# Kernel tuning notes

Hardware: AMD Instinct MI355X
Metric: run time of the kernel (lower is better)

The kernel has to match this reference:

```python
import jax, jax.numpy as jnp
import numpy as np

N = 1024
H = 1024
B, T = 64, 256


def setup_inputs() -> dict:
    key = jax.random.key(0)
    ks = jax.random.split(key, 12)
    inp = {
        "h_time": jax.random.normal(ks[0], (B, T, H), dtype=jnp.float32),
        "A_pearson": jax.random.uniform(ks[1], (N, N), dtype=jnp.float32),
        "E_dyn": jax.random.normal(ks[2], (N, H), dtype=jnp.float32) * 0.1,
        "alpha_raw": jnp.float32(0.5),
        "tau_raw": jnp.float32(1.0),
        # gate_gen: Linear(H, H//2) -> GELU -> Linear(H//2, N) -> Sigmoid
        "gate_W1": jax.random.normal(ks[3], (H, H // 2), dtype=jnp.float32) * (1.0 / np.sqrt(H)),
        "gate_b1": jnp.zeros((H // 2,), dtype=jnp.float32),
        "gate_W2": jax.random.normal(ks[4], (H // 2, N), dtype=jnp.float32) * (1.0 / np.sqrt(H // 2)),
        "gate_b2": jnp.zeros((N,), dtype=jnp.float32),
        "h2n_W": jax.random.normal(ks[5], (H, N), dtype=jnp.float32) * (1.0 / np.sqrt(H)),
        "h2n_b": jnp.zeros((N,), dtype=jnp.float32),
        "n2h_W": jax.random.normal(ks[6], (N, H), dtype=jnp.float32) * (1.0 / np.sqrt(N)),
        "n2h_b": jnp.zeros((H,), dtype=jnp.float32),
        "ln_w": jnp.ones((H,), dtype=jnp.float32),
        "ln_b": jnp.zeros((H,), dtype=jnp.float32),
    }
    return inp


def _layernorm(x, w, b, eps=1e-5):
    mu = x.mean(-1, keepdims=True)
    var = ((x - mu) ** 2).mean(-1, keepdims=True)
    return (x - mu) * jax.lax.rsqrt(var + eps) * w + b


def reference(h_time, A_pearson, E_dyn, alpha_raw, tau_raw,
              gate_W1, gate_b1, gate_W2, gate_b2,
              h2n_W, h2n_b, n2h_W, n2h_b, ln_w, ln_b):
    tau = jax.nn.softplus(tau_raw) + 1e-6
    alpha = jax.nn.sigmoid(alpha_raw)

    h_mean = h_time.mean(axis=(0, 1))                      # [H]
    E = E_dyn + h_mean[None, :]
    E_cur = E / jnp.maximum(jnp.linalg.norm(E, axis=-1, keepdims=True), 1e-12)  # F.normalize

    A_dyn = jax.nn.relu(E_cur @ E_cur.T)                   # [N,N]
    A_dyn = A_dyn / (A_dyn.sum(axis=-1, keepdims=True) + 1e-6)
    A_dyn = 0.5 * (A_dyn + A_dyn.T)
    A_base = alpha * A_pearson + (1.0 - alpha) * A_dyn

    h_gate = h_time.mean(axis=1)                           # [B,H]
    hid = jax.nn.gelu(h_gate @ gate_W1 + gate_b1, approximate=False)
    gamma = jax.nn.sigmoid(hid @ gate_W2 + gate_b2)        # [B,N]

    # Python loop over batch == row-scaling by mean gate
    A_mix = A_base * gamma.mean(axis=0)[:, None]           # [N,N]

    z_nodes = h_time @ h2n_W + h2n_b                       # [B,T,N]
    z_gcn = jnp.einsum('btn,mn->btm', z_nodes, A_mix)      # z_nodes @ A_mix.T
    msg_h = z_gcn @ n2h_W + n2h_b                          # [B,T,H]

    logits = (A_base @ E_cur) / tau                        # [N,H]
    node_attn = jax.nn.softmax(logits, axis=0)
    global_w = jnp.tanh(node_attn.mean(axis=0))            # [H]

    y = h_time * (1.0 + global_w) + msg_h
    return _layernorm(y, ln_w, ln_b)
```

## Files before the change

### kernel.cpp

```cpp
#include <hip/hip_runtime.h>
#include <math.h>

#define H 1024
#define Nn 1024
#define Bb 64
#define Tt 256
#define BT (Bb * Tt)

typedef unsigned short ushort_t;
typedef __attribute__((ext_vector_type(8))) short bf16x8;
typedef __attribute__((ext_vector_type(4))) float f32x4;


__device__ __forceinline__ ushort_t f2bf(float x) {
    union { float f; unsigned u; } v; v.f = x;
    unsigned r = v.u + 0x7FFFu + ((v.u >> 16) & 1u);
    return (ushort_t)(r >> 16);
}
__device__ __forceinline__ float bf2f(ushort_t h) {
    union { unsigned u; float f; } v; v.u = ((unsigned)h) << 16; return v.f;
}

__device__ __forceinline__ float block_reduce_sum_256(float v) {
    __shared__ float sbuf[4];
    __syncthreads();
    #pragma unroll
    for (int off = 32; off > 0; off >>= 1) v += __shfl_down(v, off, 64);
    int lane = threadIdx.x & 63, w = threadIdx.x >> 6;
    if (lane == 0) sbuf[w] = v;
    __syncthreads();
    if (threadIdx.x == 0) sbuf[0] = sbuf[0] + sbuf[1] + sbuf[2] + sbuf[3];
    __syncthreads();
    return sbuf[0];
}


__global__ void k_hgate(const float* __restrict__ h_time, float* __restrict__ h_gate,
                        ushort_t* __restrict__ ht_bf16, const float* __restrict__ n2h_b,
                        float* __restrict__ rowsumS, float* __restrict__ bias_h) {
    int b = blockIdx.y;
    int col = blockIdx.x * 256 + threadIdx.x;
    if (b == 0) {
        rowsumS[col] = 0.f;
        bias_h[col] = n2h_b[col];
    }
    float s = 0.f;
    const size_t base = (size_t)b * Tt * H + col;
    for (int t = 0; t < Tt; ++t) {
        float v = h_time[base + (size_t)t * H];
        s += v;
        ht_bf16[base + (size_t)t * H] = f2bf(v);
    }
    h_gate[b * H + col] = s * (1.0f / Tt);
}

__global__ void k_hmean(const float* __restrict__ h_gate, float* __restrict__ h_mean) {
    int h = blockIdx.x * 256 + threadIdx.x;
    float s = 0.f;
    for (int b = 0; b < Bb; ++b) s += h_gate[b * H + h];
    h_mean[h] = s * (1.0f / Bb);
}

__global__ void k_ecur(const float* __restrict__ E_dyn, const float* __restrict__ h_mean,
                       ushort_t* __restrict__ E_b) {
    int n = blockIdx.x;
    float e[4]; float ss = 0.f;
    #pragma unroll
    for (int q = 0; q < 4; ++q) {
        int h = threadIdx.x + 256 * q;
        e[q] = E_dyn[(size_t)n * H + h] + h_mean[h];
        ss += e[q] * e[q];
    }
    float tot = block_reduce_sum_256(ss);
    float scale = 1.0f / fmaxf(sqrtf(tot), 1e-12f);
    #pragma unroll
    for (int q = 0; q < 4; ++q) {
        int h = threadIdx.x + 256 * q;
        E_b[(size_t)n * H + h] = f2bf(e[q] * scale);
    }
}

__global__ void k_prepW(const float* __restrict__ n2h_W, const float* __restrict__ h2n_W,
                        const float* __restrict__ W1, const float* __restrict__ W2,
                        ushort_t* __restrict__ n2hWT_h, ushort_t* __restrict__ n2hWT_l,
                        ushort_t* __restrict__ h2nW_h, ushort_t* __restrict__ h2nW_l,
                        float* __restrict__ W1T, float* __restrict__ W2T) {
    __shared__ float tile[32][33];
    int id = blockIdx.x;
    int tx = threadIdx.x & 31, ty = threadIdx.x >> 5;
    if (id < 1024) {
        int i0 = (id >> 5) * 32, j0 = (id & 31) * 32;
        #pragma unroll
        for (int q = 0; q < 4; ++q)
            tile[ty + 8 * q][tx] = n2h_W[(size_t)(i0 + ty + 8 * q) * H + j0 + tx];
        __syncthreads();
        #pragma unroll
        for (int q = 0; q < 4; ++q) {
            float v = tile[tx][ty + 8 * q];
            size_t o = (size_t)(j0 + ty + 8 * q) * Nn + i0 + tx;
            ushort_t hh = f2bf(v);
            n2hWT_h[o] = hh;
            n2hWT_l[o] = f2bf(v - bf2f(hh));
        }
    } else if (id < 2048) {
        size_t idx = (size_t)(id - 1024) * 1024 + threadIdx.x * 4;
        float4 v = *(const float4*)&h2n_W[idx];
        float c[4] = {v.x, v.y, v.z, v.w};
        union { ushort_t u[4]; uint2 w; } ph, pl;
        #pragma unroll
        for (int q = 0; q < 4; ++q) {
            ph.u[q] = f2bf(c[q]);
            pl.u[q] = f2bf(c[q] - bf2f(ph.u[q]));
        }
        *(uint2*)&h2nW_h[idx] = ph.w;
        *(uint2*)&h2nW_l[idx] = pl.w;
    } else if (id < 2560) {
        int t = id - 2048;
        int i0 = (t >> 4) * 32, j0 = (t & 15) * 32;
        #pragma unroll
        for (int q = 0; q < 4; ++q)
            tile[ty + 8 * q][tx] = W1[(size_t)(i0 + ty + 8 * q) * 512 + j0 + tx];
        __syncthreads();
        #pragma unroll
        for (int q = 0; q < 4; ++q)
            W1T[(size_t)(j0 + ty + 8 * q) * 1024 + i0 + tx] = tile[tx][ty + 8 * q];
    } else {
        int t = id - 2560;
        int i0 = (t >> 5) * 32, j0 = (t & 31) * 32;
        #pragma unroll
        for (int q = 0; q < 4; ++q)
            tile[ty + 8 * q][tx] = W2[(size_t)(i0 + ty + 8 * q) * 1024 + j0 + tx];
        __syncthreads();
        #pragma unroll
        for (int q = 0; q < 4; ++q)
            W2T[(size_t)(j0 + ty + 8 * q) * 512 + i0 + tx] = tile[tx][ty + 8 * q];
    }
}

__global__ __launch_bounds__(256) void k_mlp1(const float* __restrict__ h_gate,
                                              const float* __restrict__ W1T,
                                              const float* __restrict__ b1,
                                              float* __restrict__ hid) {
    int gid = blockIdx.x * 4 + (threadIdx.x >> 6);
    int lane = threadIdx.x & 63;
    int b = gid >> 9, j = gid & 511;
    const float* xr = h_gate + b * H;
    const float* wr = W1T + (size_t)j * H;
    float s = 0.f;
    #pragma unroll
    for (int it = 0; it < 4; ++it) {
        int k = it * 256 + lane * 4;
        float4 x4 = *(const float4*)&xr[k];
        float4 w4 = *(const float4*)&wr[k];
        s += x4.x * w4.x + x4.y * w4.y + x4.z * w4.z + x4.w * w4.w;
    }
    #pragma unroll
    for (int off = 32; off > 0; off >>= 1) s += __shfl_down(s, off, 64);
    if (lane == 0) {
        float a = s + b1[j];
        hid[b * 512 + j] = 0.5f * a * (1.0f + erff(a * 0.70710678118654752f));
    }
}

__global__ __launch_bounds__(256) void k_mlp2(const float* __restrict__ hid,
                                              const float* __restrict__ W2T,
                                              const float* __restrict__ b2,
                                              float* __restrict__ gmean) {
    int n = blockIdx.x * 4 + (threadIdx.x >> 6);
    int lane = threadIdx.x & 63;
    const float* wr = W2T + (size_t)n * 512;
    float4 w0 = *(const float4*)&wr[lane * 4];
    float4 w1 = *(const float4*)&wr[256 + lane * 4];
    float bb = b2[n];
    float acc = 0.f;
    for (int b = 0; b < Bb; ++b) {
        const float* xr = hid + b * 512;
        float4 x0 = *(const float4*)&xr[lane * 4];
        float4 x1 = *(const float4*)&xr[256 + lane * 4];
        float s = x0.x * w0.x + x0.y * w0.y + x0.z * w0.z + x0.w * w0.w
                + x1.x * w1.x + x1.y * w1.y + x1.z * w1.z + x1.w * w1.w;
        #pragma unroll
        for (int off = 32; off > 0; off >>= 1) s += __shfl_down(s, off, 64);
        if (lane == 0) acc += 1.0f / (1.0f + expf(-(s + bb)));
    }
    if (lane == 0) gmean[n] = acc * (1.0f / Bb);
}

__global__ void k_amixT(const ushort_t* __restrict__ Sb, const float* __restrict__ A_p,
                        const float* __restrict__ rowsumS, const float* __restrict__ gmean,
                        const float* __restrict__ alpha_raw,
                        ushort_t* __restrict__ Th, ushort_t* __restrict__ Tl) {
    __shared__ float tile[32][33];
    int i0 = blockIdx.y * 32, j0 = blockIdx.x * 32;
    int tx = threadIdx.x & 31, ty = threadIdx.x >> 5;
    float alpha = 1.0f / (1.0f + expf(-alpha_raw[0]));
    #pragma unroll
    for (int q = 0; q < 4; ++q) {
        int i = i0 + ty + 8 * q, j = j0 + tx;
        size_t idx = (size_t)i * Nn + j;
        float s = bf2f(Sb[idx]);
        float ad = 0.5f * s * (1.0f / (rowsumS[i] + 1e-6f) + 1.0f / (rowsumS[j] + 1e-6f));
        tile[ty + 8 * q][tx] = gmean[i] * fmaf(alpha, A_p[idx], (1.0f - alpha) * ad);
    }
    __syncthreads();
    #pragma unroll
    for (int q = 0; q < 4; ++q) {
        float v = tile[tx][ty + 8 * q];
        size_t o = (size_t)(j0 + ty + 8 * q) * Nn + i0 + tx;
        ushort_t hh = f2bf(v);
        Th[o] = hh;
        Tl[o] = f2bf(v - bf2f(hh));
    }
}

template <int PASSES, int EPI>
__global__ __launch_bounds__(256) void gemm64_bt(
    const ushort_t* __restrict__ Ah, const ushort_t* __restrict__ Al,
    const ushort_t* __restrict__ Bh, const ushort_t* __restrict__ Bl,
    ushort_t* __restrict__ O1, ushort_t* __restrict__ O2,
    float* __restrict__ fout, const float* __restrict__ fvec,
    int M, int N, int K) {
    constexpr int NST = (PASSES == 3) ? 4 : 2;
    __shared__ ushort_t sStage[NST * 64 * 32];
    ushort_t* sAh = sStage;
    ushort_t* sBh = sStage + 64 * 32;
    ushort_t* sAl = sStage + (NST == 4 ? 2 * 64 * 32 : 0);
    ushort_t* sBl = sStage + (NST == 4 ? 3 * 64 * 32 : 0);
    const int tid = threadIdx.x, wave = tid >> 6, lane = tid & 63;
    const int quad = lane >> 4, l16 = lane & 15;
    const int m0 = blockIdx.y * 64, n0 = blockIdx.x * 64;
    const int wm = (wave >> 1) * 32, wn = (wave & 1) * 32;

    f32x4 acc[2][2];
    #pragma unroll
    for (int i = 0; i < 2; ++i)
        #pragma unroll
        for (int j = 0; j < 2; ++j)
            acc[i][j] = (f32x4){0.f, 0.f, 0.f, 0.f};

    for (int k0 = 0; k0 < K; k0 += 32) {
        __syncthreads();
        {
            const int row = tid >> 2, q = tid & 3;
            const size_t offA = (size_t)(m0 + row) * K + k0 + q * 8;
            const size_t offB = (size_t)(n0 + row) * K + k0 + q * 8;
            __builtin_amdgcn_global_load_lds(
                (const __attribute__((address_space(1))) unsigned int*)(Ah + offA),
                (__attribute__((address_space(3))) unsigned int*)&sAh[tid * 8], 16, 0, 0);
            __builtin_amdgcn_global_load_lds(
                (const __attribute__((address_space(1))) unsigned int*)(Bh + offB),
                (__attribute__((address_space(3))) unsigned int*)&sBh[tid * 8], 16, 0, 0);
            if constexpr (PASSES == 3) {
                __builtin_amdgcn_global_load_lds(
                    (const __attribute__((address_space(1))) unsigned int*)(Al + offA),
                    (__attribute__((address_space(3))) unsigned int*)&sAl[tid * 8], 16, 0, 0);
                __builtin_amdgcn_global_load_lds(
                    (const __attribute__((address_space(1))) unsigned int*)(Bl + offB),
                    (__attribute__((address_space(3))) unsigned int*)&sBl[tid * 8], 16, 0, 0);
            }
        }
        __syncthreads();
        bf16x8 fah[2], fbh[2];
        bf16x8 fal[PASSES == 3 ? 2 : 1], fbl[PASSES == 3 ? 2 : 1];
        #pragma unroll
        for (int i = 0; i < 2; ++i) {
            fah[i] = *(const bf16x8*)&sAh[(wm + i * 16 + l16) * 32 + quad * 8];
            fbh[i] = *(const bf16x8*)&sBh[(wn + i * 16 + l16) * 32 + quad * 8];
            if constexpr (PASSES == 3) {
                fal[i] = *(const bf16x8*)&sAl[(wm + i * 16 + l16) * 32 + quad * 8];
                fbl[i] = *(const bf16x8*)&sBl[(wn + i * 16 + l16) * 32 + quad * 8];
            }
        }
        #pragma unroll
        for (int i = 0; i < 2; ++i)
            #pragma unroll
            for (int j = 0; j < 2; ++j) {
                acc[i][j] = __builtin_amdgcn_mfma_f32_16x16x32_bf16(fah[i], fbh[j], acc[i][j], 0, 0, 0);
                if constexpr (PASSES == 3) {
                    acc[i][j] = __builtin_amdgcn_mfma_f32_16x16x32_bf16(fah[i], fbl[j], acc[i][j], 0, 0, 0);
                    acc[i][j] = __builtin_amdgcn_mfma_f32_16x16x32_bf16(fal[i], fbh[j], acc[i][j], 0, 0, 0);
                }
            }
    }

    float fv[2];
    if constexpr (EPI == 2) {
        #pragma unroll
        for (int j = 0; j < 2; ++j) fv[j] = fvec[n0 + wn + j * 16 + l16];
    }
    #pragma unroll
    for (int i = 0; i < 2; ++i)
        #pragma unroll
        for (int r = 0; r < 4; ++r) {
            const int m = m0 + wm + i * 16 + quad * 4 + r;
            float rowacc = 0.f;
            #pragma unroll
            for (int j = 0; j < 2; ++j) {
                const size_t o = (size_t)m * N + n0 + wn + j * 16 + l16;
                float v = acc[i][j][r];
                if constexpr (EPI == 1) {
                    v = fmaxf(v, 0.f);
                    O1[o] = f2bf(v);
                    rowacc += v;
                } else if constexpr (EPI == 2) {
                    ushort_t hh = f2bf(v);
                    O1[o] = hh;
                    O2[o] = f2bf(v - bf2f(hh));
                    rowacc += v * fv[j];
                } else {
                    O1[o] = f2bf(v);
                }
            }
            if constexpr (EPI == 1 || EPI == 2) {
                rowacc += __shfl_xor(rowacc, 1);
                rowacc += __shfl_xor(rowacc, 2);
                rowacc += __shfl_xor(rowacc, 4);
                rowacc += __shfl_xor(rowacc, 8);
                if (l16 == 0) atomicAdd(&fout[m], rowacc);
            }
        }
}

__global__ __launch_bounds__(256) void gemm_big(
    const ushort_t* __restrict__ A, const ushort_t* __restrict__ Bt,
    float* __restrict__ fout, const float* __restrict__ fvec,
    int M, int N, int K) {
    __shared__ ushort_t sStage[2 * 128 * 32];
    ushort_t* sAh = sStage;
    ushort_t* sBh = sStage + 128 * 32;

    const int tid = threadIdx.x;
    const int wave = tid >> 6, lane = tid & 63;
    const int quad = lane >> 4, l16 = lane & 15;
    int bx = blockIdx.x, g = bx & 7, s = bx >> 3;
    const int m0 = (g * 16 + (s >> 3)) * 128;
    const int n0 = (s & 7) * 128;
    const int wm = (wave >> 1) * 64, wn = (wave & 1) * 64;

    f32x4 acc[4][4];
    #pragma unroll
    for (int i = 0; i < 4; ++i)
        #pragma unroll
        for (int j = 0; j < 4; ++j)
            acc[i][j] = (f32x4){0.f, 0.f, 0.f, 0.f};

    for (int k0 = 0; k0 < K; k0 += 32) {
        __syncthreads();
        #pragma unroll
        for (int inst = 0; inst < 2; ++inst) {
            const int cbase = (wave * 2 + inst) * 64;
            const int c = cbase + lane;
            const int row = c >> 2, q = c & 3;
            const size_t offA = (size_t)(m0 + row) * K + k0 + q * 8;
            const size_t offB = (size_t)(n0 + row) * K + k0 + q * 8;
            __builtin_amdgcn_global_load_lds(
                (const __attribute__((address_space(1))) unsigned int*)(A + offA),
                (__attribute__((address_space(3))) unsigned int*)&sAh[cbase * 8], 16, 0, 0);
            __builtin_amdgcn_global_load_lds(
                (const __attribute__((address_space(1))) unsigned int*)(Bt + offB),
                (__attribute__((address_space(3))) unsigned int*)&sBh[cbase * 8], 16, 0, 0);
        }
        __syncthreads();
        bf16x8 fah[4], fbh[4];
        #pragma unroll
        for (int i = 0; i < 4; ++i) {
            fah[i] = *(const bf16x8*)&sAh[(wm + i * 16 + l16) * 32 + quad * 8];
            fbh[i] = *(const bf16x8*)&sBh[(wn + i * 16 + l16) * 32 + quad * 8];
        }
        #pragma unroll
        for (int i = 0; i < 4; ++i)
            #pragma unroll
            for (int j = 0; j < 4; ++j)
                acc[i][j] = __builtin_amdgcn_mfma_f32_16x16x32_bf16(fah[i], fbh[j], acc[i][j], 0, 0, 0);
    }
    __syncthreads();

    float* EsW = (float*)sStage + wave * (16 * 64);
    const float SC = 1.0009765622f;

    #pragma unroll
    for (int i = 0; i < 4; ++i) {
        #pragma unroll
        for (int j = 0; j < 4; ++j)
            #pragma unroll
            for (int r = 0; r < 4; ++r)
                EsW[(quad * 4 + r) * 64 + j * 16 + l16] = acc[i][j][r];
        __syncthreads();
        #pragma unroll
        for (int it = 0; it < 4; ++it) {
            const int idx = it * 64 + lane;
            const int row = idx >> 4, f4 = idx & 15;
            const int m = m0 + wm + i * 16 + row;
            const int coln = n0 + wn + f4 * 4;
            float4 v = *(const float4*)&EsW[row * 64 + f4 * 4];
            float4 b4 = *(const float4*)&fvec[coln];
            ushort4 h4 = *(const ushort4*)&A[(size_t)m * N + coln];
            float4 y;
            y.x = v.x + b4.x + SC * bf2f(h4.x);
            y.y = v.y + b4.y + SC * bf2f(h4.y);
            y.z = v.z + b4.z + SC * bf2f(h4.z);
            y.w = v.w + b4.w + SC * bf2f(h4.w);
            *(float4*)&fout[(size_t)m * N + coln] = y;
        }
        __syncthreads();
    }
}

__global__ void k_final_ln(const float* __restrict__ ln_w, const float* __restrict__ ln_b,
                           float* __restrict__ out) {
    size_t base = (size_t)blockIdx.x * H;
    int t4 = threadIdx.x * 4;
    float4 y4 = *(const float4*)&out[base + t4];
    float mu = block_reduce_sum_256(y4.x + y4.y + y4.z + y4.w) * (1.0f / H);
    float dx = y4.x - mu, dy = y4.y - mu, dz = y4.z - mu, dw = y4.w - mu;
    float var = block_reduce_sum_256(dx * dx + dy * dy + dz * dz + dw * dw) * (1.0f / H);
    float rstd = rsqrtf(var + 1e-5f);
    float4 w4 = *(const float4*)&ln_w[t4];
    float4 b4 = *(const float4*)&ln_b[t4];
    float4 o;
    o.x = fmaf(dx * rstd, w4.x, b4.x);
    o.y = fmaf(dy * rstd, w4.y, b4.y);
    o.z = fmaf(dz * rstd, w4.z, b4.z);
    o.w = fmaf(dw * rstd, w4.w, b4.w);
    *(float4*)&out[base + t4] = o;
}


extern "C" void kernel_launch(void* const* d_in, const int* in_sizes, int n_in,
                              void* d_out, int out_size, void* d_ws, size_t ws_size,
                              hipStream_t stream) {
    const float* h_time    = (const float*)d_in[0];
    const float* A_p       = (const float*)d_in[1];
    const float* E_dyn     = (const float*)d_in[2];
    const float* alpha_raw = (const float*)d_in[3];
    const float* gW1   = (const float*)d_in[5];
    const float* gb1   = (const float*)d_in[6];
    const float* gW2   = (const float*)d_in[7];
    const float* gb2   = (const float*)d_in[8];
    const float* h2n_W = (const float*)d_in[9];
    const float* h2n_b = (const float*)d_in[10];
    const float* n2h_W = (const float*)d_in[11];
    const float* n2h_b = (const float*)d_in[12];
    const float* ln_w  = (const float*)d_in[13];
    const float* ln_b  = (const float*)d_in[14];
    float* out = (float*)d_out;

    float* ws = (float*)d_ws;
    float* h_gate  = ws;  ws += Bb * H;
    float* h_mean  = ws;  ws += H;
    float* rowsumS = ws;  ws += Nn;
    float* bias_h  = ws;  ws += H;
    float* hid     = ws;  ws += Bb * 512;
    float* gmean   = ws;  ws += Nn;
    float* W1T     = ws;  ws += 512 * H;
    float* W2T     = ws;  ws += H * 512;
    ws += 256;
    ushort_t* E_b     = (ushort_t*)ws;  ws += (Nn * H) / 2;
    ushort_t* Sb      = (ushort_t*)ws;  ws += (Nn * Nn) / 2;
    ushort_t* AmixT_h = (ushort_t*)ws;  ws += (Nn * Nn) / 2;
    ushort_t* AmixT_l = (ushort_t*)ws;  ws += (Nn * Nn) / 2;
    ushort_t* n2hWT_h = (ushort_t*)ws;  ws += (Nn * H) / 2;
    ushort_t* n2hWT_l = (ushort_t*)ws;  ws += (Nn * H) / 2;
    ushort_t* h2nW_h  = (ushort_t*)ws;  ws += (H * Nn) / 2;
    ushort_t* h2nW_l  = (ushort_t*)ws;  ws += (H * Nn) / 2;
    ushort_t* C1Th    = (ushort_t*)ws;  ws += (H * Nn) / 2;
    ushort_t* C1Tl    = (ushort_t*)ws;  ws += (H * Nn) / 2;
    ushort_t* C2t     = (ushort_t*)ws;  ws += (H * H) / 2;
    ushort_t* ht      = (ushort_t*)ws;  ws += ((size_t)BT * H) / 2;

    k_hgate<<<dim3(4, 64), 256, 0, stream>>>(h_time, h_gate, ht, n2h_b, rowsumS, bias_h);
    k_prepW<<<3072, 256, 0, stream>>>(n2h_W, h2n_W, gW1, gW2,
                                      n2hWT_h, n2hWT_l, h2nW_h, h2nW_l, W1T, W2T);
    k_hmean<<<4, 256, 0, stream>>>(h_gate, h_mean);
    k_ecur<<<1024, 256, 0, stream>>>(E_dyn, h_mean, E_b);
    k_mlp1<<<8192, 256, 0, stream>>>(h_gate, W1T, gb1, hid);
    k_mlp2<<<256, 256, 0, stream>>>(hid, W2T, gb2, gmean);
    gemm64_bt<1, 1><<<dim3(16, 16), 256, 0, stream>>>(
        E_b, nullptr, E_b, nullptr, Sb, nullptr, rowsumS, nullptr, Nn, Nn, H);
    k_amixT<<<dim3(32, 32), 256, 0, stream>>>(Sb, A_p, rowsumS, gmean, alpha_raw, AmixT_h, AmixT_l);
    gemm64_bt<3, 2><<<dim3(16, 16), 256, 0, stream>>>(
        n2hWT_h, n2hWT_l, AmixT_h, AmixT_l, C1Th, C1Tl, bias_h, h2n_b, Nn, Nn, Nn);
    gemm64_bt<3, 3><<<dim3(16, 16), 256, 0, stream>>>(
        C1Th, C1Tl, h2nW_h, h2nW_l, C2t, nullptr, nullptr, nullptr, Nn, Nn, Nn);
    gemm_big<<<1024, 256, 0, stream>>>(ht, C2t, out, bias_h, BT, H, H);
    k_final_ln<<<BT, 256, 0, stream>>>(ln_w, ln_b, out);
}
```

Before: 366.2 us.

## Merge small prep kernels, widen GEMM K-tile to 64, warp-per-row layernorm

Several independent prep kernels are merged into multi-role launches (h_time stats with weight prep, E normalization with MLP1, MLP2 with the similarity GEMM). The h_time reduction is split across 8 time chunks so more blocks share the work. Both GEMMs now stage 64-wide K tiles in shared memory, halving the number of barrier and load rounds at the cost of more LDS per block. The final layernorm handles one row per wavefront with shuffle reductions instead of block-level shared memory. Together these aim to cut launch overhead, raise parallelism in the bandwidth-bound prep, and reduce sync cost, but the larger LDS footprint may lower occupancy.

Result: faster. 346.6 us (-5.4%).

```diff
diff --git a/kernel.cpp b/kernel.cpp
--- a/kernel.cpp
+++ b/kernel.cpp
@@ -34,62 +34,39 @@
     return sbuf[0];
 }
 
-
-__global__ void k_hgate(const float* __restrict__ h_time, float* __restrict__ h_gate,
-                        ushort_t* __restrict__ ht_bf16, const float* __restrict__ n2h_b,
-                        float* __restrict__ rowsumS, float* __restrict__ bias_h) {
-    int b = blockIdx.y;
-    int col = blockIdx.x * 256 + threadIdx.x;
-    if (b == 0) {
-        rowsumS[col] = 0.f;
-        bias_h[col] = n2h_b[col];
-    }
-    float s = 0.f;
-    const size_t base = (size_t)b * Tt * H + col;
-    for (int t = 0; t < Tt; ++t) {
-        float v = h_time[base + (size_t)t * H];
-        s += v;
-        ht_bf16[base + (size_t)t * H] = f2bf(v);
-    }
-    h_gate[b * H + col] = s * (1.0f / Tt);
-}
-
-__global__ void k_hmean(const float* __restrict__ h_gate, float* __restrict__ h_mean) {
-    int h = blockIdx.x * 256 + threadIdx.x;
-    float s = 0.f;
-    for (int b = 0; b < Bb; ++b) s += h_gate[b * H + h];
-    h_mean[h] = s * (1.0f / Bb);
-}
-
-__global__ void k_ecur(const float* __restrict__ E_dyn, const float* __restrict__ h_mean,
-                       ushort_t* __restrict__ E_b) {
-    int n = blockIdx.x;
-    float e[4]; float ss = 0.f;
-    #pragma unroll
-    for (int q = 0; q < 4; ++q) {
-        int h = threadIdx.x + 256 * q;
-        e[q] = E_dyn[(size_t)n * H + h] + h_mean[h];
-        ss += e[q] * e[q];
-    }
-    float tot = block_reduce_sum_256(ss);
-    float scale = 1.0f / fmaxf(sqrtf(tot), 1e-12f);
-    #pragma unroll
-    for (int q = 0; q < 4; ++q) {
-        int h = threadIdx.x + 256 * q;
-        E_b[(size_t)n * H + h] = f2bf(e[q] * scale);
-    }
-}
-
-__global__ void k_prepW(const float* __restrict__ n2h_W, const float* __restrict__ h2n_W,
-                        const float* __restrict__ W1, const float* __restrict__ W2,
-                        ushort_t* __restrict__ n2hWT_h, ushort_t* __restrict__ n2hWT_l,
-                        ushort_t* __restrict__ h2nW_h, ushort_t* __restrict__ h2nW_l,
-                        float* __restrict__ W1T, float* __restrict__ W2T) {
+__global__ void k_stage1(const float* __restrict__ h_time, float* __restrict__ hg_part,
+                         ushort_t* __restrict__ ht_bf16, const float* __restrict__ n2h_b,
+                         float* __restrict__ rowsumS, float* __restrict__ bias_h,
+                         const float* __restrict__ n2h_W, const float* __restrict__ h2n_W,
+                         const float* __restrict__ W1, const float* __restrict__ W2,
+                         ushort_t* __restrict__ n2hWT_h, ushort_t* __restrict__ n2hWT_l,
+                         ushort_t* __restrict__ h2nW_h, ushort_t* __restrict__ h2nW_l,
+                         float* __restrict__ W1T, float* __restrict__ W2T) {
     __shared__ float tile[32][33];
     int id = blockIdx.x;
+    if (id < 2048) {
+        int b = id >> 5, r = id & 31;
+        int z = r >> 2, cb = r & 3;
+        int col = cb * 256 + threadIdx.x;
+        if (b == 0 && z == 0) {
+            rowsumS[col] = 0.f;
+            bias_h[col] = n2h_b[col];
+        }
+        float s = 0.f;
+        #pragma unroll 4
+        for (int t = z * 32; t < z * 32 + 32; ++t) {
+            size_t o = ((size_t)b * Tt + t) * H + col;
+            float v = h_time[o];
+            s += v;
+            ht_bf16[o] = f2bf(v);
+        }
+        hg_part[(size_t)(b * 8 + z) * H + col] = s;
+        return;
+    }
     int tx = threadIdx.x & 31, ty = threadIdx.x >> 5;
-    if (id < 1024) {
-        int i0 = (id >> 5) * 32, j0 = (id & 31) * 32;
+    if (id < 3072) {
+        int t = id - 2048;
+        int i0 = (t >> 5) * 32, j0 = (t & 31) * 32;
         #pragma unroll
         for (int q = 0; q < 4; ++q)
             tile[ty + 8 * q][tx] = n2h_W[(size_t)(i0 + ty + 8 * q) * H + j0 + tx];
@@ -102,8 +79,8 @@
             n2hWT_h[o] = hh;
             n2hWT_l[o] = f2bf(v - bf2f(hh));
         }
-    } else if (id < 2048) {
-        size_t idx = (size_t)(id - 1024) * 1024 + threadIdx.x * 4;
+    } else if (id < 4096) {
+        size_t idx = (size_t)(id - 3072) * 1024 + threadIdx.x * 4;
         float4 v = *(const float4*)&h2n_W[idx];
         float c[4] = {v.x, v.y, v.z, v.w};
         union { ushort_t u[4]; uint2 w; } ph, pl;
@@ -114,8 +91,8 @@
         }
         *(uint2*)&h2nW_h[idx] = ph.w;
         *(uint2*)&h2nW_l[idx] = pl.w;
-    } else if (id < 2560) {
-        int t = id - 2048;
+    } else if (id < 4608) {
+        int t = id - 4096;
         int i0 = (t >> 4) * 32, j0 = (t & 15) * 32;
         #pragma unroll
         for (int q = 0; q < 4; ++q)
@@ -125,7 +102,7 @@
         for (int q = 0; q < 4; ++q)
             W1T[(size_t)(j0 + ty + 8 * q) * 1024 + i0 + tx] = tile[tx][ty + 8 * q];
     } else {
-        int t = id - 2560;
+        int t = id - 4608;
         int i0 = (t >> 5) * 32, j0 = (t & 31) * 32;
         #pragma unroll
         for (int q = 0; q < 4; ++q)
@@ -137,11 +114,48 @@
     }
 }
 
-__global__ __launch_bounds__(256) void k_mlp1(const float* __restrict__ h_gate,
-                                              const float* __restrict__ W1T,
-                                              const float* __restrict__ b1,
-                                              float* __restrict__ hid) {
-    int gid = blockIdx.x * 4 + (threadIdx.x >> 6);
+__global__ void k_stage2(const float* __restrict__ hg_part, float* __restrict__ h_gate,
+                         float* __restrict__ h_mean) {
+    int id = blockIdx.x;
+    if (id < 256) {
+        int b = id >> 2, cb = id & 3;
+        int col = cb * 256 + threadIdx.x;
+        float s = 0.f;
+        #pragma unroll
+        for (int z = 0; z < 8; ++z) s += hg_part[(size_t)(b * 8 + z) * H + col];
+        h_gate[b * H + col] = s * (1.0f / Tt);
+    } else {
+        int h = (id - 256) * 256 + threadIdx.x;
+        float s = 0.f;
+        for (int r = 0; r < 512; ++r) s += hg_part[(size_t)r * H + h];
+        h_mean[h] = s * (1.0f / (Bb * Tt));
+    }
+}
+
+__global__ __launch_bounds__(256) void k_stage3(
+    const float* __restrict__ E_dyn, const float* __restrict__ h_mean,
+    ushort_t* __restrict__ E_b,
+    const float* __restrict__ h_gate, const float* __restrict__ W1T,
+    const float* __restrict__ b1, float* __restrict__ hid) {
+    if (blockIdx.x < 1024) {
+        int n = blockIdx.x;
+        float e[4]; float ss = 0.f;
+        #pragma unroll
+        for (int q = 0; q < 4; ++q) {
+            int h = threadIdx.x + 256 * q;
+            e[q] = E_dyn[(size_t)n * H + h] + h_mean[h];
+            ss += e[q] * e[q];
+        }
+        float tot = block_reduce_sum_256(ss);
+        float scale = 1.0f / fmaxf(sqrtf(tot), 1e-12f);
+        #pragma unroll
+        for (int q = 0; q < 4; ++q) {
+            int h = threadIdx.x + 256 * q;
+            E_b[(size_t)n * H + h] = f2bf(e[q] * scale);
+        }
+        return;
+    }
+    int gid = (blockIdx.x - 1024) * 4 + (threadIdx.x >> 6);
     int lane = threadIdx.x & 63;
     int b = gid >> 9, j = gid & 511;
     const float* xr = h_gate + b * H;
@@ -162,73 +176,23 @@
     }
 }
 
-__global__ __launch_bounds__(256) void k_mlp2(const float* __restrict__ hid,
-                                              const float* __restrict__ W2T,
-                                              const float* __restrict__ b2,
-                                              float* __restrict__ gmean) {
-    int n = blockIdx.x * 4 + (threadIdx.x >> 6);
-    int lane = threadIdx.x & 63;
-    const float* wr = W2T + (size_t)n * 512;
-    float4 w0 = *(const float4*)&wr[lane * 4];
-    float4 w1 = *(const float4*)&wr[256 + lane * 4];
-    float bb = b2[n];
-    float acc = 0.f;
-    for (int b = 0; b < Bb; ++b) {
-        const float* xr = hid + b * 512;
-        float4 x0 = *(const float4*)&xr[lane * 4];
-        float4 x1 = *(const float4*)&xr[256 + lane * 4];
-        float s = x0.x * w0.x + x0.y * w0.y + x0.z * w0.z + x0.w * w0.w
-                + x1.x * w1.x + x1.y * w1.y + x1.z * w1.z + x1.w * w1.w;
-        #pragma unroll
-        for (int off = 32; off > 0; off >>= 1) s += __shfl_down(s, off, 64);
-        if (lane == 0) acc += 1.0f / (1.0f + expf(-(s + bb)));
-    }
-    if (lane == 0) gmean[n] = acc * (1.0f / Bb);
-}
-
-__global__ void k_amixT(const ushort_t* __restrict__ Sb, const float* __restrict__ A_p,
-                        const float* __restrict__ rowsumS, const float* __restrict__ gmean,
-                        const float* __restrict__ alpha_raw,
-                        ushort_t* __restrict__ Th, ushort_t* __restrict__ Tl) {
-    __shared__ float tile[32][33];
-    int i0 = blockIdx.y * 32, j0 = blockIdx.x * 32;
-    int tx = threadIdx.x & 31, ty = threadIdx.x >> 5;
-    float alpha = 1.0f / (1.0f + expf(-alpha_raw[0]));
-    #pragma unroll
-    for (int q = 0; q < 4; ++q) {
-        int i = i0 + ty + 8 * q, j = j0 + tx;
-        size_t idx = (size_t)i * Nn + j;
-        float s = bf2f(Sb[idx]);
-        float ad = 0.5f * s * (1.0f / (rowsumS[i] + 1e-6f) + 1.0f / (rowsumS[j] + 1e-6f));
-        tile[ty + 8 * q][tx] = gmean[i] * fmaf(alpha, A_p[idx], (1.0f - alpha) * ad);
-    }
-    __syncthreads();
-    #pragma unroll
-    for (int q = 0; q < 4; ++q) {
-        float v = tile[tx][ty + 8 * q];
-        size_t o = (size_t)(j0 + ty + 8 * q) * Nn + i0 + tx;
-        ushort_t hh = f2bf(v);
-        Th[o] = hh;
-        Tl[o] = f2bf(v - bf2f(hh));
-    }
-}
-
 template <int PASSES, int EPI>
-__global__ __launch_bounds__(256) void gemm64_bt(
+__device__ __forceinline__ void gemm64_body(
+    int bx, int by,
     const ushort_t* __restrict__ Ah, const ushort_t* __restrict__ Al,
     const ushort_t* __restrict__ Bh, const ushort_t* __restrict__ Bl,
     ushort_t* __restrict__ O1, ushort_t* __restrict__ O2,
     float* __restrict__ fout, const float* __restrict__ fvec,
     int M, int N, int K) {
     constexpr int NST = (PASSES == 3) ? 4 : 2;
-    __shared__ ushort_t sStage[NST * 64 * 32];
+    __shared__ ushort_t sStage[NST * 64 * 64];
     ushort_t* sAh = sStage;
-    ushort_t* sBh = sStage + 64 * 32;
-    ushort_t* sAl = sStage + (NST == 4 ? 2 * 64 * 32 : 0);
-    ushort_t* sBl = sStage + (NST == 4 ? 3 * 64 * 32 : 0);
+    ushort_t* sBh = sStage + 64 * 64;
+    ushort_t* sAl = sStage + (NST == 4 ? 2 * 64 * 64 : 0);
+    ushort_t* sBl = sStage + (NST == 4 ? 3 * 64 * 64 : 0);
     const int tid = threadIdx.x, wave = tid >> 6, lane = tid & 63;
     const int quad = lane >> 4, l16 = lane & 15;
-    const int m0 = blockIdx.y * 64, n0 = blockIdx.x * 64;
+    const int m0 = by * 64, n0 = bx * 64;
     const int wm = (wave >> 1) * 32, wn = (wave & 1) * 32;
 
     f32x4 acc[2][2];
@@ -238,49 +202,56 @@
         for (int j = 0; j < 2; ++j)
             acc[i][j] = (f32x4){0.f, 0.f, 0.f, 0.f};
 
-    for (int k0 = 0; k0 < K; k0 += 32) {
-        __syncthreads();
-        {
-            const int row = tid >> 2, q = tid & 3;
+    for (int k0 = 0; k0 < K; k0 += 64) {
+        __syncthreads();
+        #pragma unroll
+        for (int inst = 0; inst < 2; ++inst) {
+            const int cbase = (wave * 2 + inst) * 64;
+            const int c = cbase + lane;
+            const int row = c >> 3, q = c & 7;
             const size_t offA = (size_t)(m0 + row) * K + k0 + q * 8;
             const size_t offB = (size_t)(n0 + row) * K + k0 + q * 8;
             __builtin_amdgcn_global_load_lds(
                 (const __attribute__((address_space(1))) unsigned int*)(Ah + offA),
-                (__attribute__((address_space(3))) unsigned int*)&sAh[tid * 8], 16, 0, 0);
+                (__attribute__((address_space(3))) unsigned int*)&sAh[cbase * 8], 16, 0, 0);
             __builtin_amdgcn_global_load_lds(
                 (const __attribute__((address_space(1))) unsigned int*)(Bh + offB),
-                (__attribute__((address_space(3))) unsigned int*)&sBh[tid * 8], 16, 0, 0);
+                (__attribute__((address_space(3))) unsigned int*)&sBh[cbase * 8], 16, 0, 0);
             if constexpr (PASSES == 3) {
                 __builtin_amdgcn_global_load_lds(
                     (const __attribute__((address_space(1))) unsigned int*)(Al + offA),
-                    (__attribute__((address_space(3))) unsigned int*)&sAl[tid * 8], 16, 0, 0);
+                    (__attribute__((address_space(3))) unsigned int*)&sAl[cbase * 8], 16, 0, 0);
                 __builtin_amdgcn_global_load_lds(
                     (const __attribute__((address_space(1))) unsigned int*)(Bl + offB),
-                    (__attribute__((address_space(3))) unsigned int*)&sBl[tid * 8], 16, 0, 0);
+                    (__attribute__((address_space(3))) unsigned int*)&sBl[cbase * 8], 16, 0, 0);
             }
         }
         __syncthreads();
-        bf16x8 fah[2], fbh[2];
-        bf16x8 fal[PASSES == 3 ? 2 : 1], fbl[PASSES == 3 ? 2 : 1];
-        #pragma unroll
-        for (int i = 0; i < 2; ++i) {
-            fah[i] = *(const bf16x8*)&sAh[(wm + i * 16 + l16) * 32 + quad * 8];
-            fbh[i] = *(const bf16x8*)&sBh[(wn + i * 16 + l16) * 32 + quad * 8];
-            if constexpr (PASSES == 3) {
-                fal[i] = *(const bf16x8*)&sAl[(wm + i * 16 + l16) * 32 + quad * 8];
-                fbl[i] = *(const bf16x8*)&sBl[(wn + i * 16 + l16) * 32 + quad * 8];
-            }
-        }
-        #pragma unroll
-        for (int i = 0; i < 2; ++i)
-            #pragma unroll
-            for (int j = 0; j < 2; ++j) {
-                acc[i][j] = __builtin_amdgcn_mfma_f32_16x16x32_bf16(fah[i], fbh[j], acc[i][j], 0, 0, 0);
+        #pragma unroll
+        for (int half = 0; half < 2; ++half) {
+            bf16x8 fah[2], fbh[2];
+            bf16x8 fal[PASSES == 3 ? 2 : 1], fbl[PASSES == 3 ? 2 : 1];
+            #pragma unroll
+            for (int i = 0; i < 2; ++i) {
+                const int ko = half * 32 + quad * 8;
+                fah[i] = *(const bf16x8*)&sAh[(wm + i * 16 + l16) * 64 + ko];
+                fbh[i] = *(const bf16x8*)&sBh[(wn + i * 16 + l16) * 64 + ko];
                 if constexpr (PASSES == 3) {
-                    acc[i][j] = __builtin_amdgcn_mfma_f32_16x16x32_bf16(fah[i], fbl[j], acc[i][j], 0, 0, 0);
-                    acc[i][j] = __builtin_amdgcn_mfma_f32_16x16x32_bf16(fal[i], fbh[j], acc[i][j], 0, 0, 0);
+                    fal[i] = *(const bf16x8*)&sAl[(wm + i * 16 + l16) * 64 + ko];
+                    fbl[i] = *(const bf16x8*)&sBl[(wn + i * 16 + l16) * 64 + ko];
                 }
             }
+            #pragma unroll
+            for (int i = 0; i < 2; ++i)
+                #pragma unroll
+                for (int j = 0; j < 2; ++j) {
+                    acc[i][j] = __builtin_amdgcn_mfma_f32_16x16x32_bf16(fah[i], fbh[j], acc[i][j], 0, 0, 0);
+                    if constexpr (PASSES == 3) {
+                        acc[i][j] = __builtin_amdgcn_mfma_f32_16x16x32_bf16(fah[i], fbl[j], acc[i][j], 0, 0, 0);
+                        acc[i][j] = __builtin_amdgcn_mfma_f32_16x16x32_bf16(fal[i], fbh[j], acc[i][j], 0, 0, 0);
+                    }
+                }
+        }
     }
 
     float fv[2];
@@ -321,13 +292,87 @@
         }
 }
 
+__global__ __launch_bounds__(256) void k_stage4(
+    const float* __restrict__ hid, const float* __restrict__ W2T,
+    const float* __restrict__ b2, float* __restrict__ gmean,
+    const ushort_t* __restrict__ E_b, ushort_t* __restrict__ Sb,
+    float* __restrict__ rowsumS) {
+    if (blockIdx.x < 256) {
+        int n = blockIdx.x * 4 + (threadIdx.x >> 6);
+        int lane = threadIdx.x & 63;
+        const float* wr = W2T + (size_t)n * 512;
+        float4 w0 = *(const float4*)&wr[lane * 4];
+        float4 w1 = *(const float4*)&wr[256 + lane * 4];
+        float bb = b2[n];
+        float acc = 0.f;
+        for (int b = 0; b < Bb; ++b) {
+            const float* xr = hid + b * 512;
+            float4 x0 = *(const float4*)&xr[lane * 4];
+            float4 x1 = *(const float4*)&xr[256 + lane * 4];
+            float s = x0.x * w0.x + x0.y * w0.y + x0.z * w0.z + x0.w * w0.w
+                    + x1.x * w1.x + x1.y * w1.y + x1.z * w1.z + x1.w * w1.w;
+            #pragma unroll
+            for (int off = 32; off > 0; off >>= 1) s += __shfl_down(s, off, 64);
+            if (lane == 0) acc += 1.0f / (1.0f + expf(-(s + bb)));
+        }
+        if (lane == 0) gmean[n] = acc * (1.0f / Bb);
+        return;
+    }
+    int t = blockIdx.x - 256;
+    gemm64_body<1, 1>(t & 15, t >> 4, E_b, nullptr, E_b, nullptr,
+                      Sb, nullptr, rowsumS, nullptr, Nn, Nn, H);
+}
+
+__global__ void k_amixT(const ushort_t* __restrict__ Sb, const float* __restrict__ A_p,
+                        const float* __restrict__ rowsumS, const float* __restrict__ gmean,
+                        const float* __restrict__ alpha_raw,
+                        ushort_t* __restrict__ Th, ushort_t* __restrict__ Tl) {
+    __shared__ float tile[32][33];
+    int i0 = blockIdx.y * 32, j0 = blockIdx.x * 32;
+    int tx = threadIdx.x & 31, ty = threadIdx.x >> 5;
+    float alpha = 1.0f / (1.0f + expf(-alpha_raw[0]));
+    #pragma unroll
+    for (int q = 0; q < 4; ++q) {
+        int i = i0 + ty + 8 * q, j = j0 + tx;
+        size_t idx = (size_t)i * Nn + j;
+        float s = bf2f(Sb[idx]);
+        float ad = 0.5f * s * (1.0f / (rowsumS[i] + 1e-6f) + 1.0f / (rowsumS[j] + 1e-6f));
+        tile[ty + 8 * q][tx] = gmean[i] * fmaf(alpha, A_p[idx], (1.0f - alpha) * ad);
+    }
+    __syncthreads();
+    #pragma unroll
+    for (int q = 0; q < 4; ++q) {
+        float v = tile[tx][ty + 8 * q];
+        size_t o = (size_t)(j0 + ty + 8 * q) * Nn + i0 + tx;
+        ushort_t hh = f2bf(v);
+        Th[o] = hh;
+        Tl[o] = f2bf(v - bf2f(hh));
+    }
+}
+
+__global__ __launch_bounds__(256) void k_c1t(
+    const ushort_t* __restrict__ Ah, const ushort_t* __restrict__ Al,
+    const ushort_t* __restrict__ Bh, const ushort_t* __restrict__ Bl,
+    ushort_t* __restrict__ O1, ushort_t* __restrict__ O2,
+    float* __restrict__ fout, const float* __restrict__ fvec) {
+    gemm64_body<3, 2>(blockIdx.x & 15, blockIdx.x >> 4, Ah, Al, Bh, Bl, O1, O2, fout, fvec,
+                      Nn, Nn, Nn);
+}
+__global__ __launch_bounds__(256) void k_c2t(
+    const ushort_t* __restrict__ Ah, const ushort_t* __restrict__ Al,
+    const ushort_t* __restrict__ Bh, const ushort_t* __restrict__ Bl,
+    ushort_t* __restrict__ O1) {
+    gemm64_body<3, 3>(blockIdx.x & 15, blockIdx.x >> 4, Ah, Al, Bh, Bl, O1, nullptr,
+                      nullptr, nullptr, Nn, Nn, Nn);
+}
+
 __global__ __launch_bounds__(256) void gemm_big(
     const ushort_t* __restrict__ A, const ushort_t* __restrict__ Bt,
     float* __restrict__ fout, const float* __restrict__ fvec,
     int M, int N, int K) {
-    __shared__ ushort_t sStage[2 * 128 * 32];
+    __shared__ ushort_t sStage[2 * 128 * 64];
     ushort_t* sAh = sStage;
-    ushort_t* sBh = sStage + 128 * 32;
+    ushort_t* sBh = sStage + 128 * 64;
 
     const int tid = threadIdx.x;
     const int wave = tid >> 6, lane = tid & 63;
@@ -344,13 +389,13 @@
         for (int j = 0; j < 4; ++j)
             acc[i][j] = (f32x4){0.f, 0.f, 0.f, 0.f};
 
-    for (int k0 = 0; k0 < K; k0 += 32) {
-        __syncthreads();
-        #pragma unroll
-        for (int inst = 0; inst < 2; ++inst) {
-            const int cbase = (wave * 2 + inst) * 64;
+    for (int k0 = 0; k0 < K; k0 += 64) {
+        __syncthreads();
+        #pragma unroll
+        for (int inst = 0; inst < 4; ++inst) {
+            const int cbase = (wave * 4 + inst) * 64;
             const int c = cbase + lane;
-            const int row = c >> 2, q = c & 3;
+            const int row = c >> 3, q = c & 7;
             const size_t offA = (size_t)(m0 + row) * K + k0 + q * 8;
             const size_t offB = (size_t)(n0 + row) * K + k0 + q * 8;
             __builtin_amdgcn_global_load_lds(
@@ -361,17 +406,21 @@
                 (__attribute__((address_space(3))) unsigned int*)&sBh[cbase * 8], 16, 0, 0);
         }
         __syncthreads();
-        bf16x8 fah[4], fbh[4];
-        #pragma unroll
-        for (int i = 0; i < 4; ++i) {
-            fah[i] = *(const bf16x8*)&sAh[(wm + i * 16 + l16) * 32 + quad * 8];
-            fbh[i] = *(const bf16x8*)&sBh[(wn + i * 16 + l16) * 32 + quad * 8];
-        }
-        #pragma unroll
-        for (int i = 0; i < 4; ++i)
-            #pragma unroll
-            for (int j = 0; j < 4; ++j)
-                acc[i][j] = __builtin_amdgcn_mfma_f32_16x16x32_bf16(fah[i], fbh[j], acc[i][j], 0, 0, 0);
+        #pragma unroll
+        for (int half = 0; half < 2; ++half) {
+            bf16x8 fah[4], fbh[4];
+            #pragma unroll
+            for (int i = 0; i < 4; ++i) {
+                const int ko = half * 32 + quad * 8;
+                fah[i] = *(const bf16x8*)&sAh[(wm + i * 16 + l16) * 64 + ko];
+                fbh[i] = *(const bf16x8*)&sBh[(wn + i * 16 + l16) * 64 + ko];
+            }
+            #pragma unroll
+            for (int i = 0; i < 4; ++i)
+                #pragma unroll
+                for (int j = 0; j < 4; ++j)
+                    acc[i][j] = __builtin_amdgcn_mfma_f32_16x16x32_bf16(fah[i], fbh[j], acc[i][j], 0, 0, 0);
+        }
     }
     __syncthreads();
 
@@ -406,23 +455,42 @@
     }
 }
 
-__global__ void k_final_ln(const float* __restrict__ ln_w, const float* __restrict__ ln_b,
-                           float* __restrict__ out) {
-    size_t base = (size_t)blockIdx.x * H;
-    int t4 = threadIdx.x * 4;
-    float4 y4 = *(const float4*)&out[base + t4];
-    float mu = block_reduce_sum_256(y4.x + y4.y + y4.z + y4.w) * (1.0f / H);
-    float dx = y4.x - mu, dy = y4.y - mu, dz = y4.z - mu, dw = y4.w - mu;
-    float var = block_reduce_sum_256(dx * dx + dy * dy + dz * dz + dw * dw) * (1.0f / H);
-    float rstd = rsqrtf(var + 1e-5f);
-    float4 w4 = *(const float4*)&ln_w[t4];
-    float4 b4 = *(const float4*)&ln_b[t4];
-    float4 o;
-    o.x = fmaf(dx * rstd, w4.x, b4.x);
-    o.y = fmaf(dy * rstd, w4.y, b4.y);
-    o.z = fmaf(dz * rstd, w4.z, b4.z);
-    o.w = fmaf(dw * rstd, w4.w, b4.w);
-    *(float4*)&out[base + t4] = o;
+__global__ __launch_bounds__(256) void k_final_ln(const float* __restrict__ ln_w,
+                                                  const float* __restrict__ ln_b,
+                                                  float* __restrict__ out) {
+    int wave = threadIdx.x >> 6, lane = threadIdx.x & 63;
+    size_t row = (size_t)blockIdx.x * 4 + wave;
+    float4 v[4];
+    float s = 0.f;
+    #pragma unroll
+    for (int q = 0; q < 4; ++q) {
+        v[q] = *(const float4*)&out[row * H + q * 256 + lane * 4];
+        s += v[q].x + v[q].y + v[q].z + v[q].w;
+    }
+    #pragma unroll
+    for (int off = 1; off < 64; off <<= 1) s += __shfl_xor(s, off, 64);
+    float mu = s * (1.0f / H);
+    float ss = 0.f;
+    #pragma unroll
+    for (int q = 0; q < 4; ++q) {
+        v[q].x -= mu; v[q].y -= mu; v[q].z -= mu; v[q].w -= mu;
+        ss += v[q].x * v[q].x + v[q].y * v[q].y + v[q].z * v[q].z + v[q].w * v[q].w;
+    }
+    #pragma unroll
+    for (int off = 1; off < 64; off <<= 1) ss += __shfl_xor(ss, off, 64);
+    float rstd = rsqrtf(ss * (1.0f / H) + 1e-5f);
+    #pragma unroll
+    for (int q = 0; q < 4; ++q) {
+        int k = q * 256 + lane * 4;
+        float4 w4 = *(const float4*)&ln_w[k];
+        float4 b4 = *(const float4*)&ln_b[k];
+        float4 o;
+        o.x = fmaf(v[q].x * rstd, w4.x, b4.x);
+        o.y = fmaf(v[q].y * rstd, w4.y, b4.y);
+        o.z = fmaf(v[q].z * rstd, w4.z, b4.z);
+        o.w = fmaf(v[q].w * rstd, w4.w, b4.w);
+        *(float4*)&out[row * H + k] = o;
+    }
 }
 
 
@@ -454,6 +522,7 @@
     float* gmean   = ws;  ws += Nn;
     float* W1T     = ws;  ws += 512 * H;
     float* W2T     = ws;  ws += H * 512;
+    float* hg_part = ws;  ws += 512 * H;
     ws += 256;
     ushort_t* E_b     = (ushort_t*)ws;  ws += (Nn * H) / 2;
     ushort_t* Sb      = (ushort_t*)ws;  ws += (Nn * Nn) / 2;
@@ -468,20 +537,15 @@
     ushort_t* C2t     = (ushort_t*)ws;  ws += (H * H) / 2;
     ushort_t* ht      = (ushort_t*)ws;  ws += ((size_t)BT * H) / 2;
 
-    k_hgate<<<dim3(4, 64), 256, 0, stream>>>(h_time, h_gate, ht, n2h_b, rowsumS, bias_h);
-    k_prepW<<<3072, 256, 0, stream>>>(n2h_W, h2n_W, gW1, gW2,
-                                      n2hWT_h, n2hWT_l, h2nW_h, h2nW_l, W1T, W2T);
-    k_hmean<<<4, 256, 0, stream>>>(h_gate, h_mean);
-    k_ecur<<<1024, 256, 0, stream>>>(E_dyn, h_mean, E_b);
-    k_mlp1<<<8192, 256, 0, stream>>>(h_gate, W1T, gb1, hid);
-    k_mlp2<<<256, 256, 0, stream>>>(hid, W2T, gb2, gmean);
-    gemm64_bt<1, 1><<<dim3(16, 16), 256, 0, stream>>>(
-        E_b, nullptr, E_b, nullptr, Sb, nullptr, rowsumS, nullptr, Nn, Nn, H);
+    k_stage1<<<5120, 256, 0, stream>>>(h_time, hg_part, ht, n2h_b, rowsumS, bias_h,
+                                       n2h_W, h2n_W, gW1, gW2,
+                                       n2hWT_h, n2hWT_l, h2nW_h, h2nW_l, W1T, W2T);
+    k_stage2<<<260, 256, 0, stream>>>(hg_part, h_gate, h_mean);
+    k_stage3<<<9216, 256, 0, stream>>>(E_dyn, h_mean, E_b, h_gate, W1T, gb1, hid);
+    k_stage4<<<512, 256, 0, stream>>>(hid, W2T, gb2, gmean, E_b, Sb, rowsumS);
     k_amixT<<<dim3(32, 32), 256, 0, stream>>>(Sb, A_p, rowsumS, gmean, alpha_raw, AmixT_h, AmixT_l);
-    gemm64_bt<3, 2><<<dim3(16, 16), 256, 0, stream>>>(
-        n2hWT_h, n2hWT_l, AmixT_h, AmixT_l, C1Th, C1Tl, bias_h, h2n_b, Nn, Nn, Nn);
-    gemm64_bt<3, 3><<<dim3(16, 16), 256, 0, stream>>>(
-        C1Th, C1Tl, h2nW_h, h2nW_l, C2t, nullptr, nullptr, nullptr, Nn, Nn, Nn);
+    k_c1t<<<256, 256, 0, stream>>>(n2hWT_h, n2hWT_l, AmixT_h, AmixT_l, C1Th, C1Tl, bias_h, h2n_b);
+    k_c2t<<<256, 256, 0, stream>>>(C1Th, C1Tl, h2nW_h, h2nW_l, C2t);
     gemm_big<<<1024, 256, 0, stream>>>(ht, C2t, out, bias_h, BT, H, H);
-    k_final_ln<<<BT, 256, 0, stream>>>(ln_w, ln_b, out);
-}
+    k_final_ln<<<4096, 256, 0, stream>>>(ln_w, ln_b, out);
+}
```
